# Kernel optimization log

Hardware: AMD Instinct MI355X
Metric: run time of the kernel (lower is better)

The kernel has to match this reference:

```python
import jax, jax.numpy as jnp
import numpy as np

HEADS = 16
HEAD_DIM = 64
NEG = 1000000000.0  # additive mask magnitude from source


def setup_inputs() -> dict:
    key = jax.random.key(0)
    ks = jax.random.split(key, 6)
    N, S, D = 4, 2048, 1024
    x = jax.random.normal(ks[0], (N, S, D), dtype=jnp.float32)
    scale = 1.0 / np.sqrt(D)
    wq = jax.random.normal(ks[1], (D, D), dtype=jnp.float32) * scale
    wk = jax.random.normal(ks[2], (D, D), dtype=jnp.float32) * scale
    wv = jax.random.normal(ks[3], (D, D), dtype=jnp.float32) * scale
    wo = jax.random.normal(ks[4], (D, D), dtype=jnp.float32) * scale
    bo = jnp.zeros((D,), dtype=jnp.float32)
    return {"x": x, "wq": wq, "wk": wk, "wv": wv, "wo": wo, "bo": bo}


def reference(x, wq, wk, wv, wo, bo):
    N, S, D = x.shape
    h, d = HEADS, HEAD_DIM
    attn_scale = 1.0 / np.sqrt(d)
    # projections (no bias, qkv_bias=False)
    q = (x @ wq.T).reshape(N, S, h, d).transpose(0, 2, 1, 3)  # N h S d
    k = (x @ wk.T).reshape(N, S, h, d).transpose(0, 2, 1, 3)  # N h S d
    v = (x @ wv.T).reshape(N, S, h, d).transpose(0, 2, 1, 3)  # N h S d
    logits = jnp.einsum('nhsd,nhtd->nhst', q, k) * attn_scale  # N h S S
    scores = jax.nn.softmax(logits, axis=-1)
    # faithful quirk: additive mask applied AFTER softmax
    # triu(ones) - 1 -> 0 on/above diagonal, -1 strictly below
    causal_mask = NEG * (jnp.triu(jnp.ones((S, S), dtype=x.dtype)) - 1.0)
    scores = scores + causal_mask  # broadcasts over N, h
    out = jnp.einsum('nhst,nhtd->nhsd', scores, v)  # N h S d
    out = out.transpose(0, 2, 1, 3).reshape(N, S, h * d)
    return out @ wo.T + bo  # dropout p=0 -> identity
```

## Files before the change

### kernel.cpp

```cpp
#include <hip/hip_runtime.h>

#define AS1 __attribute__((address_space(1)))
#define AS3 __attribute__((address_space(3)))

typedef __bf16 bf16x8 __attribute__((ext_vector_type(8)));
typedef float f32x4 __attribute__((ext_vector_type(4)));

__device__ __forceinline__ unsigned short f2bf(float f) {
  unsigned int u = __float_as_uint(f);
  return (unsigned short)((u + 0x7fffu + ((u >> 16) & 1u)) >> 16);
}

__device__ __forceinline__ void gemm_body(int bx, int by, int bz,
                                          const unsigned short* __restrict__ A,
                                          const unsigned short* __restrict__ B,
                                          float* __restrict__ C,
                                          unsigned short* __restrict__ Cb,
                                          const float* __restrict__ bias,
                                          int ldC, int K, int kchunk, int planeElems,
                                          unsigned short* lA, unsigned short* lB) {
  int tid = threadIdx.x;
  int w = tid >> 6, lane = tid & 63;
  int r0 = bx * 128, c0 = by * 128;
  int wr = w >> 1, wc = w & 1;
  int ml = lane & 15, q = lane >> 4;

  int srow = lane >> 3;
  int scol = 8 * ((lane & 7) ^ srow);
  const unsigned short* gA = A + (size_t)(r0 + 32 * w + srow) * K + scol + (size_t)bz * kchunk;
  const unsigned short* gB = B + (size_t)(c0 + 32 * w + srow) * K + scol + (size_t)bz * kchunk;
  unsigned short* lApw = lA + 32 * w * 64;
  unsigned short* lBpw = lB + 32 * w * 64;

  const f32x4 vzero = {0.f, 0.f, 0.f, 0.f};
  f32x4 acc[4][4];
#pragma unroll
  for (int mt = 0; mt < 4; ++mt)
#pragma unroll
    for (int nt = 0; nt < 4; ++nt) acc[mt][nt] = vzero;

  for (int k0 = 0; k0 < kchunk; k0 += 64) {
#pragma unroll
    for (int n = 0; n < 4; ++n) {
      __builtin_amdgcn_global_load_lds((const AS1 void*)(gA + (size_t)8 * n * K + k0),
                                       (AS3 void*)(lApw + n * 512), 16, 0, 0);
      __builtin_amdgcn_global_load_lds((const AS1 void*)(gB + (size_t)8 * n * K + k0),
                                       (AS3 void*)(lBpw + n * 512), 16, 0, 0);
    }
    __syncthreads();
#pragma unroll
    for (int h = 0; h < 2; ++h) {
      bf16x8 af[4], bfv[4];
      int kb = 4 * h + q;
#pragma unroll
      for (int mt = 0; mt < 4; ++mt) {
        int R = 64 * wr + 16 * mt + ml;
        af[mt] = *(const bf16x8*)(lA + R * 64 + 8 * (kb ^ (ml & 7)));
      }
#pragma unroll
      for (int nt = 0; nt < 4; ++nt) {
        int R = 64 * wc + 16 * nt + ml;
        bfv[nt] = *(const bf16x8*)(lB + R * 64 + 8 * (kb ^ (ml & 7)));
      }
#pragma unroll
      for (int mt = 0; mt < 4; ++mt)
#pragma unroll
        for (int nt = 0; nt < 4; ++nt)
          acc[mt][nt] = __builtin_amdgcn_mfma_f32_16x16x32_bf16(af[mt], bfv[nt], acc[mt][nt], 0, 0, 0);
    }
    __syncthreads();
  }

  if (Cb) {
#pragma unroll
    for (int nt = 0; nt < 4; ++nt) {
      int col = c0 + 64 * wc + 16 * nt + ml;
#pragma unroll
      for (int mt = 0; mt < 4; ++mt) {
        int rowb = r0 + 64 * wr + 16 * mt + q * 4;
#pragma unroll
        for (int r = 0; r < 4; ++r)
          Cb[(size_t)(rowb + r) * ldC + col] = f2bf(-1e9f * acc[mt][nt][r]);
      }
    }
  } else {
    C += (size_t)bz * planeElems;
#pragma unroll
    for (int nt = 0; nt < 4; ++nt) {
      int col = c0 + 64 * wc + 16 * nt + ml;
      float bv = bias ? bias[col] : 0.f;
#pragma unroll
      for (int mt = 0; mt < 4; ++mt) {
        int rowb = r0 + 64 * wr + 16 * mt + q * 4;
#pragma unroll
        for (int r = 0; r < 4; ++r)
          C[(size_t)(rowb + r) * ldC + col] = acc[mt][nt][r] + bv;
      }
    }
  }
}

__global__ __launch_bounds__(256) void prep_tilesum_k(const float* __restrict__ x,
                                                      const float* __restrict__ wo,
                                                      const float* __restrict__ wv,
                                                      float* __restrict__ T,
                                                      unsigned short* __restrict__ wo_b,
                                                      unsigned short* __restrict__ wvT_b) {
  __shared__ float t[32][33];
  int b = blockIdx.x;
  if (b < 128) {
    int f = threadIdx.x * 4;
    const float* p = x + (size_t)b * 65536 + f;
    float sx = 0.f, sy = 0.f, sz = 0.f, sw = 0.f;
#pragma unroll 8
    for (int i = 0; i < 64; ++i) {
      float4 v = *(const float4*)(p + (size_t)i * 1024);
      sx += v.x; sy += v.y; sz += v.z; sw += v.w;
    }
    float4 s = {sx, sy, sz, sw};
    *(float4*)(T + (size_t)b * 1024 + f) = s;
  } else if (b < 1152) {
    int i = ((b - 128) * 256 + threadIdx.x) * 4;
    float4 v = *(const float4*)(wo + i);
    ushort4 o;
    o.x = f2bf(v.x); o.y = f2bf(v.y); o.z = f2bf(v.z); o.w = f2bf(v.w);
    *(ushort4*)(wo_b + i) = o;
  } else {
    int bb = b - 1152;
    int bx = (bb & 31) * 32, by = (bb >> 5) * 32;
    int tx = threadIdx.x & 31, ty = threadIdx.x >> 5;
    for (int i = ty; i < 32; i += 8) t[i][tx] = wv[(by + i) * 1024 + bx + tx];
    __syncthreads();
    for (int i = ty; i < 32; i += 8) wvT_b[(bx + i) * 1024 + by + tx] = f2bf(t[tx][i]);
  }
}

__global__ __launch_bounds__(256) void scan_smallgemm_k(const float* __restrict__ x,
                                                        const float* __restrict__ T,
                                                        unsigned short* __restrict__ Xc,
                                                        const unsigned short* __restrict__ wo_b,
                                                        const unsigned short* __restrict__ wvT_b,
                                                        unsigned short* __restrict__ Mp) {
  __shared__ unsigned short lA[128 * 64];
  __shared__ unsigned short lB[128 * 64];
  int b = blockIdx.x;
  if (b < 64) {
    gemm_body(b & 7, b >> 3, 0, wo_b, wvT_b, nullptr, Mp, nullptr,
              1024, 1024, 1024, 0, lA, lB);
  } else {
    int bt = b - 64;
    int tile = bt & 31, b0 = bt - tile;
    int f = threadIdx.x * 4;
    float ax = 0.f, ay = 0.f, az = 0.f, aw = 0.f;
#pragma unroll 4
    for (int t2 = 0; t2 < tile; ++t2) {
      float4 v = *(const float4*)(T + (size_t)(b0 + t2) * 1024 + f);
      ax += v.x; ay += v.y; az += v.z; aw += v.w;
    }
    const float* px = x + (size_t)bt * 65536 + f;
    unsigned short* po = Xc + (size_t)bt * 65536 + f;
#pragma unroll 4
    for (int i = 0; i < 64; ++i) {
      uint2 pk;
      pk.x = (unsigned int)f2bf(ax) | ((unsigned int)f2bf(ay) << 16);
      pk.y = (unsigned int)f2bf(az) | ((unsigned int)f2bf(aw) << 16);
      *(uint2*)(po + (size_t)i * 1024) = pk;
      float4 v = *(const float4*)(px + (size_t)i * 1024);
      ax += v.x; ay += v.y; az += v.z; aw += v.w;
    }
  }
}

__global__ __launch_bounds__(256) void gemm_big_k(const unsigned short* __restrict__ A,
                                                  const unsigned short* __restrict__ B,
                                                  float* __restrict__ C,
                                                  const float* __restrict__ bias) {
  __shared__ unsigned short lA[128 * 64];
  __shared__ unsigned short lB[128 * 64];
  int p = blockIdx.x;
  int l = (p & 7) * 64 + (p >> 3);
  gemm_body(l >> 3, l & 7, 0, A, B, C, nullptr, bias,
            1024, 1024, 1024, 0, lA, lB);
}

extern "C" void kernel_launch(void* const* d_in, const int* in_sizes, int n_in,
                              void* d_out, int out_size, void* d_ws, size_t ws_size,
                              hipStream_t stream) {
  const float* x  = (const float*)d_in[0];
  const float* wv = (const float*)d_in[3];
  const float* wo = (const float*)d_in[4];
  const float* bo = (const float*)d_in[5];
  char* ws = (char*)d_ws;

  unsigned short* wo_b  = (unsigned short*)ws;
  unsigned short* wvT_b = (unsigned short*)(ws + (2u << 20));
  unsigned short* Mp    = (unsigned short*)(ws + (4u << 20));
  float*          Tsum  = (float*)(ws + (6u << 20));
  unsigned short* Xc    = (unsigned short*)(ws + (7u << 20));

  prep_tilesum_k<<<2176, 256, 0, stream>>>(x, wo, wv, Tsum, wo_b, wvT_b);
  scan_smallgemm_k<<<192, 256, 0, stream>>>(x, Tsum, Xc, wo_b, wvT_b, Mp);
  gemm_big_k<<<512, 256, 0, stream>>>(Xc, Mp, (float*)d_out, bo);
}
```

Baseline: 139.9 us.

## Fuse three kernels into one cooperative kernel with grid-wide syncs

Replaces the three separate launches (prep/tile-sum, scan plus small GEMM, big GEMM) with a single cooperative kernel of 512 blocks that separates the phases with grid.sync(). The per-phase work is redistributed across the fixed 512-block grid, with each block handling more elements or tiles, so that all blocks stay resident. The goal is to remove inter-kernel launch gaps and tail effects. In exchange it adds two grid barriers, requires two blocks per CU for residency, and leaves many blocks idle during the smaller phases.

```diff
diff --git a/kernel.cpp b/kernel.cpp
--- a/kernel.cpp
+++ b/kernel.cpp
@@ -1,4 +1,7 @@
 #include <hip/hip_runtime.h>
+#include <hip/hip_cooperative_groups.h>
+
+namespace cg = cooperative_groups;
 
 #define AS1 __attribute__((address_space(1)))
 #define AS3 __attribute__((address_space(3)))
@@ -11,13 +14,13 @@
   return (unsigned short)((u + 0x7fffu + ((u >> 16) & 1u)) >> 16);
 }
 
-__device__ __forceinline__ void gemm_body(int bx, int by, int bz,
+__device__ __forceinline__ void gemm_body(int bx, int by,
                                           const unsigned short* __restrict__ A,
                                           const unsigned short* __restrict__ B,
                                           float* __restrict__ C,
                                           unsigned short* __restrict__ Cb,
                                           const float* __restrict__ bias,
-                                          int ldC, int K, int kchunk, int planeElems,
+                                          int ldC, int K,
                                           unsigned short* lA, unsigned short* lB) {
   int tid = threadIdx.x;
   int w = tid >> 6, lane = tid & 63;
@@ -27,8 +30,8 @@
 
   int srow = lane >> 3;
   int scol = 8 * ((lane & 7) ^ srow);
-  const unsigned short* gA = A + (size_t)(r0 + 32 * w + srow) * K + scol + (size_t)bz * kchunk;
-  const unsigned short* gB = B + (size_t)(c0 + 32 * w + srow) * K + scol + (size_t)bz * kchunk;
+  const unsigned short* gA = A + (size_t)(r0 + 32 * w + srow) * K + scol;
+  const unsigned short* gB = B + (size_t)(c0 + 32 * w + srow) * K + scol;
   unsigned short* lApw = lA + 32 * w * 64;
   unsigned short* lBpw = lB + 32 * w * 64;
 
@@ -39,7 +42,7 @@
 #pragma unroll
     for (int nt = 0; nt < 4; ++nt) acc[mt][nt] = vzero;
 
-  for (int k0 = 0; k0 < kchunk; k0 += 64) {
+  for (int k0 = 0; k0 < K; k0 += 64) {
 #pragma unroll
     for (int n = 0; n < 4; ++n) {
       __builtin_amdgcn_global_load_lds((const AS1 void*)(gA + (size_t)8 * n * K + k0),
@@ -84,11 +87,10 @@
       }
     }
   } else {
-    C += (size_t)bz * planeElems;
 #pragma unroll
     for (int nt = 0; nt < 4; ++nt) {
       int col = c0 + 64 * wc + 16 * nt + ml;
-      float bv = bias ? bias[col] : 0.f;
+      float bv = bias[col];
 #pragma unroll
       for (int mt = 0; mt < 4; ++mt) {
         int rowb = r0 + 64 * wr + 16 * mt + q * 4;
@@ -100,87 +102,81 @@
   }
 }
 
-__global__ __launch_bounds__(256) void prep_tilesum_k(const float* __restrict__ x,
-                                                      const float* __restrict__ wo,
-                                                      const float* __restrict__ wv,
-                                                      float* __restrict__ T,
-                                                      unsigned short* __restrict__ wo_b,
-                                                      unsigned short* __restrict__ wvT_b) {
-  __shared__ float t[32][33];
+__global__ __launch_bounds__(256, 2) void fused_all_k(
+    const float* __restrict__ x, const float* __restrict__ wv,
+    const float* __restrict__ wo, const float* __restrict__ bo,
+    float* __restrict__ out, float* __restrict__ T,
+    unsigned short* __restrict__ wo_b, unsigned short* __restrict__ wvT_b,
+    unsigned short* __restrict__ Mp, unsigned short* __restrict__ Xc) {
+  __shared__ unsigned short lA[128 * 64];
+  __shared__ unsigned short lB[128 * 64];
+  cg::grid_group grid = cg::this_grid();
   int b = blockIdx.x;
-  if (b < 128) {
-    int f = threadIdx.x * 4;
-    const float* p = x + (size_t)b * 65536 + f;
-    float sx = 0.f, sy = 0.f, sz = 0.f, sw = 0.f;
+  int tid = threadIdx.x;
+
+  if (b < 256) {
+    int bt = b >> 1;
+    int f = (b & 1) * 512 + tid * 2;
+    const float* p = x + (size_t)bt * 65536 + f;
+    float sx = 0.f, sy = 0.f;
 #pragma unroll 8
     for (int i = 0; i < 64; ++i) {
-      float4 v = *(const float4*)(p + (size_t)i * 1024);
-      sx += v.x; sy += v.y; sz += v.z; sw += v.w;
-    }
-    float4 s = {sx, sy, sz, sw};
-    *(float4*)(T + (size_t)b * 1024 + f) = s;
-  } else if (b < 1152) {
-    int i = ((b - 128) * 256 + threadIdx.x) * 4;
-    float4 v = *(const float4*)(wo + i);
-    ushort4 o;
-    o.x = f2bf(v.x); o.y = f2bf(v.y); o.z = f2bf(v.z); o.w = f2bf(v.w);
-    *(ushort4*)(wo_b + i) = o;
+      float2 v = *(const float2*)(p + (size_t)i * 1024);
+      sx += v.x; sy += v.y;
+    }
+    float2 s = {sx, sy};
+    *(float2*)(T + (size_t)bt * 1024 + f) = s;
+  } else if (b < 384) {
+#pragma unroll
+    for (int j = 0; j < 8; ++j) {
+      int i = (b - 256) * 8192 + j * 1024 + tid * 4;
+      float4 v = *(const float4*)(wo + i);
+      ushort4 o;
+      o.x = f2bf(v.x); o.y = f2bf(v.y); o.z = f2bf(v.z); o.w = f2bf(v.w);
+      *(ushort4*)(wo_b + i) = o;
+    }
   } else {
-    int bb = b - 1152;
-    int bx = (bb & 31) * 32, by = (bb >> 5) * 32;
-    int tx = threadIdx.x & 31, ty = threadIdx.x >> 5;
-    for (int i = ty; i < 32; i += 8) t[i][tx] = wv[(by + i) * 1024 + bx + tx];
-    __syncthreads();
-    for (int i = ty; i < 32; i += 8) wvT_b[(bx + i) * 1024 + by + tx] = f2bf(t[tx][i]);
-  }
-}
-
-__global__ __launch_bounds__(256) void scan_smallgemm_k(const float* __restrict__ x,
-                                                        const float* __restrict__ T,
-                                                        unsigned short* __restrict__ Xc,
-                                                        const unsigned short* __restrict__ wo_b,
-                                                        const unsigned short* __restrict__ wvT_b,
-                                                        unsigned short* __restrict__ Mp) {
-  __shared__ unsigned short lA[128 * 64];
-  __shared__ unsigned short lB[128 * 64];
-  int b = blockIdx.x;
+    float (*t)[33] = (float (*)[33])lA;
+    int tx = tid & 31, ty = tid >> 5;
+#pragma unroll
+    for (int j = 0; j < 8; ++j) {
+      int tile = (b - 384) * 8 + j;
+      int bx2 = (tile & 31) * 32, by2 = (tile >> 5) * 32;
+      for (int i = ty; i < 32; i += 8) t[i][tx] = wv[(by2 + i) * 1024 + bx2 + tx];
+      __syncthreads();
+      for (int i = ty; i < 32; i += 8) wvT_b[(bx2 + i) * 1024 + by2 + tx] = f2bf(t[tx][i]);
+      __syncthreads();
+    }
+  }
+  grid.sync();
+
   if (b < 64) {
-    gemm_body(b & 7, b >> 3, 0, wo_b, wvT_b, nullptr, Mp, nullptr,
-              1024, 1024, 1024, 0, lA, lB);
-  } else {
-    int bt = b - 64;
+    gemm_body(b & 7, b >> 3, wo_b, wvT_b, nullptr, Mp, nullptr, 1024, 1024, lA, lB);
+  } else if (b < 320) {
+    int sb = b - 64;
+    int bt = sb >> 1;
     int tile = bt & 31, b0 = bt - tile;
-    int f = threadIdx.x * 4;
-    float ax = 0.f, ay = 0.f, az = 0.f, aw = 0.f;
+    int f = (sb & 1) * 512 + tid * 2;
+    float ax = 0.f, ay = 0.f;
 #pragma unroll 4
     for (int t2 = 0; t2 < tile; ++t2) {
-      float4 v = *(const float4*)(T + (size_t)(b0 + t2) * 1024 + f);
-      ax += v.x; ay += v.y; az += v.z; aw += v.w;
+      float2 v = *(const float2*)(T + (size_t)(b0 + t2) * 1024 + f);
+      ax += v.x; ay += v.y;
     }
     const float* px = x + (size_t)bt * 65536 + f;
     unsigned short* po = Xc + (size_t)bt * 65536 + f;
 #pragma unroll 4
     for (int i = 0; i < 64; ++i) {
-      uint2 pk;
-      pk.x = (unsigned int)f2bf(ax) | ((unsigned int)f2bf(ay) << 16);
-      pk.y = (unsigned int)f2bf(az) | ((unsigned int)f2bf(aw) << 16);
-      *(uint2*)(po + (size_t)i * 1024) = pk;
-      float4 v = *(const float4*)(px + (size_t)i * 1024);
-      ax += v.x; ay += v.y; az += v.z; aw += v.w;
-    }
-  }
-}
-
-__global__ __launch_bounds__(256) void gemm_big_k(const unsigned short* __restrict__ A,
-                                                  const unsigned short* __restrict__ B,
-                                                  float* __restrict__ C,
-                                                  const float* __restrict__ bias) {
-  __shared__ unsigned short lA[128 * 64];
-  __shared__ unsigned short lB[128 * 64];
-  int p = blockIdx.x;
-  int l = (p & 7) * 64 + (p >> 3);
-  gemm_body(l >> 3, l & 7, 0, A, B, C, nullptr, bias,
-            1024, 1024, 1024, 0, lA, lB);
+      unsigned int pk = (unsigned int)f2bf(ax) | ((unsigned int)f2bf(ay) << 16);
+      *(unsigned int*)(po + (size_t)i * 1024) = pk;
+      float2 v = *(const float2*)(px + (size_t)i * 1024);
+      ax += v.x; ay += v.y;
+    }
+  }
+  grid.sync();
+
+  int l = (b & 7) * 64 + (b >> 3);
+  gemm_body(l >> 3, l & 7, Xc, Mp, out, nullptr, bo, 1024, 1024, lA, lB);
 }
 
 extern "C" void kernel_launch(void* const* d_in, const int* in_sizes, int n_in,
@@ -197,8 +193,9 @@
   unsigned short* Mp    = (unsigned short*)(ws + (4u << 20));
   float*          Tsum  = (float*)(ws + (6u << 20));
   unsigned short* Xc    = (unsigned short*)(ws + (7u << 20));
-
-  prep_tilesum_k<<<2176, 256, 0, stream>>>(x, wo, wv, Tsum, wo_b, wvT_b);
-  scan_smallgemm_k<<<192, 256, 0, stream>>>(x, Tsum, Xc, wo_b, wvT_b, Mp);
-  gemm_big_k<<<512, 256, 0, stream>>>(Xc, Mp, (float*)d_out, bo);
-}
+  float*          out   = (float*)d_out;
+
+  void* args[] = {(void*)&x, (void*)&wv, (void*)&wo, (void*)&bo, (void*)&out,
+                  (void*)&Tsum, (void*)&wo_b, (void*)&wvT_b, (void*)&Mp, (void*)&Xc};
+  hipLaunchCooperativeKernel((void*)fused_all_k, dim3(512), dim3(256), args, 0, stream);
+}
```

Result: slower. 283.3 us (+102.6%).
